# Performance work log

Hardware: AMD Instinct MI355X
Metric: run time of the kernel (lower is better)

The kernel has to match this reference:

```python
import jax, jax.numpy as jnp
import numpy as np

N_NODES = 50000
N_EDGES = 1600000
D_FEAT = 128
EPS = 1e-12  # matches F.normalize clamp_min eps


def setup_inputs() -> dict:
    key = jax.random.key(0)
    k1, k2 = jax.random.split(key)
    x = jax.random.normal(k1, (N_NODES, D_FEAT), dtype=jnp.float32)
    beta = jnp.ones((1,), dtype=jnp.float32)  # AGNNConv learnable scalar, init 1.0
    edge_index = jax.random.randint(k2, (2, N_EDGES), 0, N_NODES, dtype=jnp.int64)
    return {"x": x, "beta": beta, "edge_index": edge_index}


def reference(x, beta, edge_index):
    N = x.shape[0]
    # AGNNConv default add_self_loops=True
    loop = jnp.arange(N, dtype=edge_index.dtype)
    src = jnp.concatenate([edge_index[0], loop])  # j (source / message sender)
    dst = jnp.concatenate([edge_index[1], loop])  # i (target / aggregator)

    # cosine-similarity attention logits per edge, scaled by beta
    xn = x * jax.lax.rsqrt(jnp.maximum(jnp.sum(x * x, axis=-1, keepdims=True), EPS * EPS))
    logits = beta[0] * jnp.sum(xn[src] * xn[dst], axis=-1)  # [E+N]

    # segment softmax over incoming edges of each target node
    m = jax.ops.segment_max(logits, dst, num_segments=N)
    m = jax.lax.stop_gradient(m)
    e = jnp.exp(logits - m[dst])
    s = jax.ops.segment_sum(e, dst, num_segments=N)
    alpha = e / s[dst]  # self-loops guarantee s > 0

    # scatter-aggregate messages alpha_e * x_src
    out = jax.ops.segment_sum(alpha[:, None] * x[src], dst, num_segments=N)

    # wrapper: activation (relu); normalization=False; dropout p=0 -> identity
    return jax.nn.relu(out)
```

## Files before the change

### kernel.cpp

```cpp
#include <hip/hip_runtime.h>

#define NN 50000
#define NE 1600000
#define DF 128
#define NB 1250
#define BSZ 40
#define CAP 1664
#define NWGP 256
#define CHKP 6250
#define NBF 3125

typedef float v2f __attribute__((ext_vector_type(2)));
typedef float v4f __attribute__((ext_vector_type(4)));
typedef unsigned int v2u __attribute__((ext_vector_type(2)));

static __device__ __forceinline__ float bflo(unsigned int u) {
    unsigned int v = u << 16; float f; __builtin_memcpy(&f, &v, 4); return f;
}
static __device__ __forceinline__ float bfhi(unsigned int u) {
    unsigned int v = u & 0xFFFF0000u; float f; __builtin_memcpy(&f, &v, 4); return f;
}
static __device__ __forceinline__ unsigned int f2bf(float f) {
    unsigned int u; __builtin_memcpy(&u, &f, 4);
    u += 0x7FFFu + ((u >> 16) & 1u);
    return u >> 16;
}
static __device__ __forceinline__ v4f cvt4_i8(unsigned int u) {
    v4f r;
    r.x = (float)(int)(signed char)(u);
    r.y = (float)(int)(signed char)(u >> 8);
    r.z = (float)(int)(signed char)(u >> 16);
    r.w = (float)(int)(signed char)(u >> 24);
    return r;
}
static __device__ __forceinline__ v2f pk_fma(v2f a, v2f b, v2f c) {
    v2f d;
    asm("v_pk_fma_f32 %0, %1, %2, %3" : "=v"(d) : "v"(a), "v"(b), "0"(c));
    return d;
}
static __device__ __forceinline__ v2f pk_mul(v2f a, v2f b) {
    v2f d;
    asm("v_pk_mul_f32 %0, %1, %2" : "=v"(d) : "v"(a), "v"(b));
    return d;
}
static __device__ __forceinline__ v2f pk_add(v2f a, v2f b) {
    v2f d;
    asm("v_pk_add_f32 %0, %1, %2" : "=v"(d) : "v"(a), "v"(b));
    return d;
}

static __device__ __forceinline__ int block_excl_scan512(int v, int t, int* wsum8) {
    int lane = t & 63, wv = t >> 6;
    int s = v;
    #pragma unroll
    for (int off = 1; off < 64; off <<= 1) {
        int u = __shfl_up(s, off);
        if (lane >= off) s += u;
    }
    if (lane == 63) wsum8[wv] = s;
    __syncthreads();
    int add = 0;
    #pragma unroll
    for (int w = 0; w < 8; ++w) add += (w < wv) ? wsum8[w] : 0;
    __syncthreads();
    return s + add - v;
}

static __device__ __forceinline__ int block_excl_scan256(int v, int t, int* wsum4) {
    int lane = t & 63, wv = t >> 6;
    int s = v;
    #pragma unroll
    for (int off = 1; off < 64; off <<= 1) {
        int u = __shfl_up(s, off);
        if (lane >= off) s += u;
    }
    if (lane == 63) wsum4[wv] = s;
    __syncthreads();
    int add = 0;
    #pragma unroll
    for (int w = 0; w < 4; ++w) add += (w < wv) ? wsum4[w] : 0;
    __syncthreads();
    return s + add - v;
}

__global__ __launch_bounds__(512)
void k_norm_part(const float* __restrict__ x,
                 const int* __restrict__ ei,
                 unsigned int* __restrict__ xq,
                 float* __restrict__ norm,
                 unsigned int* __restrict__ sn,
                 unsigned int* __restrict__ descG,
                 unsigned int* __restrict__ pairs) {
    __shared__ int wsum8[8];
    __shared__ int cntL[NB];
    __shared__ int offL[NB];
    __shared__ unsigned int stg[CHKP];
    int t = threadIdx.x;
    if (blockIdx.x >= NWGP) {
        int l32 = t & 31;
        int node = (blockIdx.x - NWGP) * 16 + (t >> 5);
        float4 v = ((const float4*)(x + (size_t)node * DF))[l32];
        float ss = v.x * v.x + v.y * v.y + v.z * v.z + v.w * v.w;
        float am = fmaxf(fmaxf(fabsf(v.x), fabsf(v.y)), fmaxf(fabsf(v.z), fabsf(v.w)));
        #pragma unroll
        for (int m = 1; m < 32; m <<= 1) {
            ss += __shfl_xor(ss, m);
            am = fmaxf(am, __shfl_xor(am, m));
        }
        float rinv = rsqrtf(fmaxf(ss, 1e-24f));
        am = fmaxf(am, 1e-30f);
        float qsc = 127.0f / am;
        int q0 = (int)rintf(v.x * qsc);
        int q1 = (int)rintf(v.y * qsc);
        int q2 = (int)rintf(v.z * qsc);
        int q3 = (int)rintf(v.w * qsc);
        unsigned int u = (q0 & 255) | ((q1 & 255) << 8) | ((q2 & 255) << 16)
                       | ((unsigned int)q3 << 24);
        xq[(size_t)node * 32 + l32] = u;
        if (l32 == 0) {
            float m = am * (1.0f / 127.0f);
            float s = rinv * m;
            norm[node] = ss * rinv;
            sn[node] = (f2bf(m) << 16) | f2bf(s);
        }
        return;
    }
    int wg = blockIdx.x;
    const int* srcp = ei + wg * CHKP;
    const int* dstp = ei + NE + wg * CHKP;
    for (int i = t; i < NB; i += 512) cntL[i] = 0;
    __syncthreads();
    #pragma unroll 4
    for (int i = t; i < CHKP; i += 512) atomicAdd(&cntL[dstp[i] / BSZ], 1);
    __syncthreads();
    {
        int base = t * 3;
        int loc[3];
        int s = 0;
        #pragma unroll
        for (int q = 0; q < 3; ++q) {
            int idx = base + q;
            int v = (idx < NB) ? cntL[idx] : 0;
            loc[q] = s;
            s += v;
        }
        int ex = block_excl_scan512(s, t, wsum8);
        #pragma unroll
        for (int q = 0; q < 3; ++q) {
            int idx = base + q;
            if (idx < NB) offL[idx] = ex + loc[q];
        }
    }
    __syncthreads();
    for (int i = t; i < NB; i += 512)
        descG[(size_t)wg * NB + i] = ((unsigned int)offL[i] << 16) | (unsigned int)cntL[i];
    __syncthreads();
    #pragma unroll 2
    for (int i = t; i < CHKP; i += 512) {
        int src = srcp[i];
        int dst = dstp[i];
        int b = dst / BSZ;
        int pos = atomicAdd(&offL[b], 1);
        stg[pos] = ((unsigned int)(dst - b * BSZ) << 16) | (unsigned int)src;
    }
    __syncthreads();
    unsigned int* chunk = pairs + (size_t)wg * CHKP;
    #pragma unroll 4
    for (int i = t; i < CHKP; i += 512) chunk[i] = stg[i];
}

__global__ __launch_bounds__(256)
void k_build_gather(const unsigned int* __restrict__ xq,
                    const unsigned int* __restrict__ sn,
                    const float* __restrict__ norm,
                    const unsigned int* __restrict__ descG,
                    const unsigned int* __restrict__ pairs,
                    const float* __restrict__ beta_p,
                    float* __restrict__ out) {
    __shared__ int wsum4[4];
    __shared__ int lenS[NWGP], offS[NWGP], rbase[NWGP];
    __shared__ unsigned int rawL[CAP];
    __shared__ unsigned int colSrc[CAP];
    __shared__ unsigned int colSN[CAP];
    __shared__ int hist[BSZ];
    __shared__ int rp[BSZ + 1];
    __shared__ int stot;
    int b = blockIdx.x, t = threadIdx.x;

    {
        unsigned int d = descG[(size_t)t * NB + b];
        int len = (int)(d & 0xFFFFu);
        int ex = block_excl_scan256(len, t, wsum4);
        lenS[t] = len;
        offS[t] = (int)(d >> 16);
        rbase[t] = ex;
        if (t == 255) stot = ex + len;
    }
    if (t < BSZ) hist[t] = 0;
    __syncthreads();
    int cnt = stot;
    if (cnt > CAP) cnt = CAP;

    int g8 = t >> 3, l8 = t & 7;
    for (int r = g8; r < NWGP; r += 32) {
        int len = lenS[r];
        int rb = rbase[r];
        const unsigned int* sp = pairs + (size_t)r * CHKP + offS[r];
        for (int q = l8; q < len; q += 8) {
            int pos = rb + q;
            if (pos < CAP) rawL[pos] = sp[q];
        }
    }
    __syncthreads();
    for (int i = t; i < cnt; i += 256) atomicAdd(&hist[rawL[i] >> 16], 1);
    __syncthreads();
    if (t < 64) {
        int v = (t < BSZ) ? hist[t] : 0;
        int s = v;
        #pragma unroll
        for (int off = 1; off < 64; off <<= 1) {
            int u = __shfl_up(s, off);
            if (t >= off) s += u;
        }
        if (t < BSZ) { rp[t + 1] = s; hist[t] = s - v; }
        if (t == 0) rp[0] = 0;
    }
    __syncthreads();
    for (int i = t; i < cnt; i += 256) {
        unsigned int p = rawL[i];
        unsigned int src = p & 0xFFFFu;
        int pos = atomicAdd(&hist[p >> 16], 1);
        colSrc[pos] = src;
        colSN[pos] = sn[src];
    }
    __syncthreads();

    int lane = t & 63;
    int w = t >> 6;
    int j = lane & 15;
    int g = lane >> 4;
    float beta = beta_p[0];
    float c = -fabsf(beta);
    for (int ln = w; ln < BSZ; ln += 4) {
        int node = b * BSZ + ln;
        v2u du = ((const v2u*)(xq + (size_t)node * 32))[j];
        v4f c0 = cvt4_i8(du.x), c1 = cvt4_i8(du.y);
        v2f xd2[4];
        xd2[0].x = c0.x; xd2[0].y = c0.y;
        xd2[1].x = c0.z; xd2[1].y = c0.w;
        xd2[2].x = c1.x; xd2[2].y = c1.y;
        xd2[3].x = c1.z; xd2[3].y = c1.w;
        float sd = bflo(sn[node]);
        float ke = beta * sd;
        v2f acc2[4];
        #pragma unroll
        for (int q = 0; q < 4; ++q) { acc2[q].x = 0.f; acc2[q].y = 0.f; }
        float ssum = 0.f;
        int b0 = rp[ln], b1 = rp[ln + 1];

        int k = b0 + g;
        int kA = (k     < b1) ? k     : 0;
        int kB = (k + 4 < b1) ? k + 4 : 0;
        unsigned int srcA = colSrc[kA] & 0xFFFFu;
        unsigned int srcB = colSrc[kB] & 0xFFFFu;
        unsigned int snA = colSN[kA];
        unsigned int snB = colSN[kB];
        v2u rA = ((const v2u*)(xq + (size_t)srcA * 32))[j];
        v2u rB = ((const v2u*)(xq + (size_t)srcB * 32))[j];

        for (; k < b1; k += 8) {
            int kC = (k +  8 < b1) ? k +  8 : 0;
            int kD = (k + 12 < b1) ? k + 12 : 0;
            unsigned int srcC = colSrc[kC] & 0xFFFFu;
            unsigned int srcD = colSrc[kD] & 0xFFFFu;
            unsigned int snC = colSN[kC];
            unsigned int snD = colSN[kD];
            v2u rC = ((const v2u*)(xq + (size_t)srcC * 32))[j];
            v2u rD = ((const v2u*)(xq + (size_t)srcD * 32))[j];

            v4f a0 = cvt4_i8(rA.x), a1 = cvt4_i8(rA.y);
            v4f b0v = cvt4_i8(rB.x), b1v = cvt4_i8(rB.y);
            v2f xsA[4], xsB[4];
            xsA[0].x = a0.x; xsA[0].y = a0.y;  xsA[1].x = a0.z; xsA[1].y = a0.w;
            xsA[2].x = a1.x; xsA[2].y = a1.y;  xsA[3].x = a1.z; xsA[3].y = a1.w;
            xsB[0].x = b0v.x; xsB[0].y = b0v.y; xsB[1].x = b0v.z; xsB[1].y = b0v.w;
            xsB[2].x = b1v.x; xsB[2].y = b1v.y; xsB[3].x = b1v.z; xsB[3].y = b1v.w;
            v2f dpA = pk_mul(xd2[0], xsA[0]);
            v2f dpB = pk_mul(xd2[0], xsB[0]);
            #pragma unroll
            for (int q = 1; q < 4; ++q) {
                dpA = pk_fma(xd2[q], xsA[q], dpA);
                dpB = pk_fma(xd2[q], xsB[q], dpB);
            }
            v2f dAB;
            dAB.x = dpA.x + dpA.y;
            dAB.y = dpB.x + dpB.y;
            #pragma unroll
            for (int m = 1; m < 16; m <<= 1) {
                v2f o;
                o.x = __shfl_xor(dAB.x, m);
                o.y = __shfl_xor(dAB.y, m);
                dAB = pk_add(dAB, o);
            }
            float eA = __expf(fmaf(ke * bflo(snA), dAB.x, c));
            float eB = __expf(fmaf(ke * bflo(snB), dAB.y, c));
            eB = (k + 4 < b1) ? eB : 0.f;
            ssum += eA + eB;
            float wA = eA * bfhi(snA);
            float wB = eB * bfhi(snB);
            v2f wA2; wA2.x = wA; wA2.y = wA;
            v2f wB2; wB2.x = wB; wB2.y = wB;
            #pragma unroll
            for (int q = 0; q < 4; ++q) {
                acc2[q] = pk_fma(wA2, xsA[q], acc2[q]);
                acc2[q] = pk_fma(wB2, xsB[q], acc2[q]);
            }
            srcA = srcC; srcB = srcD; snA = snC; snB = snD; rA = rC; rB = rD;
        }

        ssum += __shfl_xor(ssum, 16);
        ssum += __shfl_xor(ssum, 32);
        #pragma unroll
        for (int q = 0; q < 4; ++q) {
            v2f o;
            o.x = __shfl_xor(acc2[q].x, 16);
            o.y = __shfl_xor(acc2[q].y, 16);
            acc2[q] = pk_add(acc2[q], o);
            o.x = __shfl_xor(acc2[q].x, 32);
            o.y = __shfl_xor(acc2[q].y, 32);
            acc2[q] = pk_add(acc2[q], o);
        }
        float e_self = __expf(beta + c);
        ssum += e_self;
        float wsl = e_self * norm[node] * sd;
        v2f wsl2; wsl2.x = wsl; wsl2.y = wsl;
        #pragma unroll
        for (int q = 0; q < 4; ++q) acc2[q] = pk_fma(wsl2, xd2[q], acc2[q]);

        if (g == 0) {
            float inv = 1.0f / ssum;
            float4 o0, o1;
            o0.x = fmaxf(0.f, acc2[0].x * inv); o0.y = fmaxf(0.f, acc2[0].y * inv);
            o0.z = fmaxf(0.f, acc2[1].x * inv); o0.w = fmaxf(0.f, acc2[1].y * inv);
            o1.x = fmaxf(0.f, acc2[2].x * inv); o1.y = fmaxf(0.f, acc2[2].y * inv);
            o1.z = fmaxf(0.f, acc2[3].x * inv); o1.w = fmaxf(0.f, acc2[3].y * inv);
            float4* op = (float4*)(out + (size_t)node * DF + 8 * j);
            op[0] = o0;
            op[1] = o1;
        }
    }
}

extern "C" void kernel_launch(void* const* d_in, const int* in_sizes, int n_in,
                              void* d_out, int out_size, void* d_ws, size_t ws_size,
                              hipStream_t stream) {
    const float* x    = (const float*)d_in[0];
    const float* beta = (const float*)d_in[1];
    const int*   ei   = (const int*)d_in[2];
    float*       out  = (float*)d_out;

    char* ws = (char*)d_ws;
    unsigned int* xq    = (unsigned int*)ws;
    float*        norm  = (float*)(ws + 6400000);
    unsigned int* sn    = (unsigned int*)(ws + 6600000);
    unsigned int* descG = (unsigned int*)(ws + 6800000);
    unsigned int* pairs = (unsigned int*)(ws + 8080000);

    k_norm_part  <<<NWGP + NBF, 512, 0, stream>>>(x, ei, xq, norm, sn, descG, pairs);
    k_build_gather<<<NB,        256, 0, stream>>>(xq, sn, norm, descG, pairs, beta, out);
}
```

Baseline: 155.9 us.

## Use offset-unsigned int8 with udot4 dot products and deeper prefetch

Stores the quantized features as unsigned bytes offset by 128 and computes each edge dot product with the hardware udot4 instruction. The offset terms are corrected using a per-node row sum stored next to the scale pair, and a weighted-sum correction is applied to the aggregation. It also merges the norm and scale arrays into one packed uint2 and deepens the software prefetch from two to four edges ahead. The aim is to cut VALU work for conversion and dot products, at the cost of more registers, extra LDS and more correction arithmetic.

```diff
diff --git a/kernel.cpp b/kernel.cpp
--- a/kernel.cpp
+++ b/kernel.cpp
@@ -11,7 +11,6 @@
 #define NBF 3125
 
 typedef float v2f __attribute__((ext_vector_type(2)));
-typedef float v4f __attribute__((ext_vector_type(4)));
 typedef unsigned int v2u __attribute__((ext_vector_type(2)));
 
 static __device__ __forceinline__ float bflo(unsigned int u) {
@@ -25,13 +24,15 @@
     u += 0x7FFFu + ((u >> 16) & 1u);
     return u >> 16;
 }
-static __device__ __forceinline__ v4f cvt4_i8(unsigned int u) {
-    v4f r;
-    r.x = (float)(int)(signed char)(u);
-    r.y = (float)(int)(signed char)(u >> 8);
-    r.z = (float)(int)(signed char)(u >> 16);
-    r.w = (float)(int)(signed char)(u >> 24);
-    return r;
+static __device__ __forceinline__ void ub8(v2u r, v2f* f) {
+    f[0].x = (float)( r.x         & 255u);
+    f[0].y = (float)((r.x >>  8)  & 255u);
+    f[1].x = (float)((r.x >> 16)  & 255u);
+    f[1].y = (float)( r.x >> 24         );
+    f[2].x = (float)( r.y         & 255u);
+    f[2].y = (float)((r.y >>  8)  & 255u);
+    f[3].x = (float)((r.y >> 16)  & 255u);
+    f[3].y = (float)( r.y >> 24         );
 }
 static __device__ __forceinline__ v2f pk_fma(v2f a, v2f b, v2f c) {
     v2f d;
@@ -87,8 +88,7 @@
 void k_norm_part(const float* __restrict__ x,
                  const int* __restrict__ ei,
                  unsigned int* __restrict__ xq,
-                 float* __restrict__ norm,
-                 unsigned int* __restrict__ sn,
+                 uint2* __restrict__ snr,
                  unsigned int* __restrict__ descG,
                  unsigned int* __restrict__ pairs) {
     __shared__ int wsum8[8];
@@ -110,18 +110,24 @@
         float rinv = rsqrtf(fmaxf(ss, 1e-24f));
         am = fmaxf(am, 1e-30f);
         float qsc = 127.0f / am;
-        int q0 = (int)rintf(v.x * qsc);
-        int q1 = (int)rintf(v.y * qsc);
-        int q2 = (int)rintf(v.z * qsc);
-        int q3 = (int)rintf(v.w * qsc);
-        unsigned int u = (q0 & 255) | ((q1 & 255) << 8) | ((q2 & 255) << 16)
-                       | ((unsigned int)q3 << 24);
+        int q0 = (int)rintf(v.x * qsc) + 128;
+        int q1 = (int)rintf(v.y * qsc) + 128;
+        int q2 = (int)rintf(v.z * qsc) + 128;
+        int q3 = (int)rintf(v.w * qsc) + 128;
+        unsigned int u = (unsigned)q0 | ((unsigned)q1 << 8) | ((unsigned)q2 << 16)
+                       | ((unsigned)q3 << 24);
+        int rs = q0 + q1 + q2 + q3;
+        #pragma unroll
+        for (int m = 1; m < 32; m <<= 1) rs += __shfl_xor(rs, m);
         xq[(size_t)node * 32 + l32] = u;
         if (l32 == 0) {
-            float m = am * (1.0f / 127.0f);
-            float s = rinv * m;
-            norm[node] = ss * rinv;
-            sn[node] = (f2bf(m) << 16) | f2bf(s);
+            float mm = am * (1.0f / 127.0f);
+            float sv = rinv * mm;
+            uint2 p;
+            p.x = (f2bf(mm) << 16) | f2bf(sv);
+            float rsf = 128.0f * (float)rs;
+            __builtin_memcpy(&p.y, &rsf, 4);
+            snr[node] = p;
         }
         return;
     }
@@ -171,8 +177,7 @@
 
 __global__ __launch_bounds__(256)
 void k_build_gather(const unsigned int* __restrict__ xq,
-                    const unsigned int* __restrict__ sn,
-                    const float* __restrict__ norm,
+                    const uint2* __restrict__ snr,
                     const unsigned int* __restrict__ descG,
                     const unsigned int* __restrict__ pairs,
                     const float* __restrict__ beta_p,
@@ -181,7 +186,7 @@
     __shared__ int lenS[NWGP], offS[NWGP], rbase[NWGP];
     __shared__ unsigned int rawL[CAP];
     __shared__ unsigned int colSrc[CAP];
-    __shared__ unsigned int colSN[CAP];
+    __shared__ uint2 colSNR[CAP];
     __shared__ int hist[BSZ];
     __shared__ int rp[BSZ + 1];
     __shared__ int stot;
@@ -231,7 +236,7 @@
         unsigned int src = p & 0xFFFFu;
         int pos = atomicAdd(&hist[p >> 16], 1);
         colSrc[pos] = src;
-        colSN[pos] = sn[src];
+        colSNR[pos] = snr[src];
     }
     __syncthreads();
 
@@ -240,61 +245,73 @@
     int j = lane & 15;
     int g = lane >> 4;
     float beta = beta_p[0];
-    float c = -fabsf(beta);
+    float cc = -fabsf(beta);
+
+#define FETCH(KK, SNV, RSV, ROW) {                                      \
+        int kc_ = ((KK) < b1r) ? (KK) : 0;                              \
+        unsigned sv_ = colSrc[kc_] & 0xFFFFu;                           \
+        uint2 tt_ = colSNR[kc_];                                        \
+        SNV = tt_.x;                                                    \
+        __builtin_memcpy(&RSV, &tt_.y, 4);                              \
+        ROW = ((const v2u*)(xq + (size_t)sv_ * 32))[j];                 \
+    }
+
     for (int ln = w; ln < BSZ; ln += 4) {
         int node = b * BSZ + ln;
         v2u du = ((const v2u*)(xq + (size_t)node * 32))[j];
-        v4f c0 = cvt4_i8(du.x), c1 = cvt4_i8(du.y);
-        v2f xd2[4];
-        xd2[0].x = c0.x; xd2[0].y = c0.y;
-        xd2[1].x = c0.z; xd2[1].y = c0.w;
-        xd2[2].x = c1.x; xd2[2].y = c1.y;
-        xd2[3].x = c1.z; xd2[3].y = c1.w;
-        float sd = bflo(sn[node]);
-        float ke = beta * sd;
+        uint2 sd = snr[node];
+        float m_d = bfhi(sd.x);
+        float s_d = bflo(sd.x);
+        float rsd; __builtin_memcpy(&rsd, &sd.y, 4);
+        float Kd = 2097152.0f - rsd;
+        float ke = beta * s_d;
+        v2f xdf[4];
+        ub8(du, xdf);
         v2f acc2[4];
         #pragma unroll
         for (int q = 0; q < 4; ++q) { acc2[q].x = 0.f; acc2[q].y = 0.f; }
-        float ssum = 0.f;
-        int b0 = rp[ln], b1 = rp[ln + 1];
-
-        int k = b0 + g;
-        int kA = (k     < b1) ? k     : 0;
-        int kB = (k + 4 < b1) ? k + 4 : 0;
-        unsigned int srcA = colSrc[kA] & 0xFFFFu;
-        unsigned int srcB = colSrc[kB] & 0xFFFFu;
-        unsigned int snA = colSN[kA];
-        unsigned int snB = colSN[kB];
-        v2u rA = ((const v2u*)(xq + (size_t)srcA * 32))[j];
-        v2u rB = ((const v2u*)(xq + (size_t)srcB * 32))[j];
-
-        for (; k < b1; k += 8) {
-            int kC = (k +  8 < b1) ? k +  8 : 0;
-            int kD = (k + 12 < b1) ? k + 12 : 0;
-            unsigned int srcC = colSrc[kC] & 0xFFFFu;
-            unsigned int srcD = colSrc[kD] & 0xFFFFu;
-            unsigned int snC = colSN[kC];
-            unsigned int snD = colSN[kD];
-            v2u rC = ((const v2u*)(xq + (size_t)srcC * 32))[j];
-            v2u rD = ((const v2u*)(xq + (size_t)srcD * 32))[j];
-
-            v4f a0 = cvt4_i8(rA.x), a1 = cvt4_i8(rA.y);
-            v4f b0v = cvt4_i8(rB.x), b1v = cvt4_i8(rB.y);
-            v2f xsA[4], xsB[4];
-            xsA[0].x = a0.x; xsA[0].y = a0.y;  xsA[1].x = a0.z; xsA[1].y = a0.w;
-            xsA[2].x = a1.x; xsA[2].y = a1.y;  xsA[3].x = a1.z; xsA[3].y = a1.w;
-            xsB[0].x = b0v.x; xsB[0].y = b0v.y; xsB[1].x = b0v.z; xsB[1].y = b0v.w;
-            xsB[2].x = b1v.x; xsB[2].y = b1v.y; xsB[3].x = b1v.z; xsB[3].y = b1v.w;
-            v2f dpA = pk_mul(xd2[0], xsA[0]);
-            v2f dpB = pk_mul(xd2[0], xsB[0]);
-            #pragma unroll
-            for (int q = 1; q < 4; ++q) {
-                dpA = pk_fma(xd2[q], xsA[q], dpA);
-                dpB = pk_fma(xd2[q], xsB[q], dpB);
+        float ssum = 0.f, wsum = 0.f;
+        int b0r = rp[ln], b1r = rp[ln + 1];
+
+        int k = b0r + g;
+        unsigned snA, snB, snC, snD, snE, snF;
+        float rsA, rsB, rsC, rsD, rsE, rsF2;
+        v2u rA, rB, rC, rD, rE, rF;
+        FETCH(k,      snA, rsA, rA);
+        FETCH(k + 4,  snB, rsB, rB);
+        FETCH(k + 8,  snC, rsC, rC);
+        FETCH(k + 12, snD, rsD, rD);
+
+        for (; k < b1r; k += 8) {
+            FETCH(k + 16, snE, rsE, rE);
+            FETCH(k + 20, snF, rsF2, rF);
+
+            v2f faA[4], faB[4];
+            ub8(rA, faA);
+            ub8(rB, faB);
+            v2f dAB;
+#if __has_builtin(__builtin_amdgcn_udot4)
+            {
+                unsigned dA = __builtin_amdgcn_udot4(du.x, rA.x,
+                              __builtin_amdgcn_udot4(du.y, rA.y, 0u, false), false);
+                unsigned dB = __builtin_amdgcn_udot4(du.x, rB.x,
+                              __builtin_amdgcn_udot4(du.y, rB.y, 0u, false), false);
+                dAB.x = (float)dA;
+                dAB.y = (float)dB;
             }
-            v2f dAB;
-            dAB.x = dpA.x + dpA.y;
-            dAB.y = dpB.x + dpB.y;
+#else
+            {
+                v2f dpA = pk_mul(xdf[0], faA[0]);
+                v2f dpB = pk_mul(xdf[0], faB[0]);
+                #pragma unroll
+                for (int q = 1; q < 4; ++q) {
+                    dpA = pk_fma(xdf[q], faA[q], dpA);
+                    dpB = pk_fma(xdf[q], faB[q], dpB);
+                }
+                dAB.x = dpA.x + dpA.y;
+                dAB.y = dpB.x + dpB.y;
+            }
+#endif
             #pragma unroll
             for (int m = 1; m < 16; m <<= 1) {
                 v2f o;
@@ -302,24 +319,32 @@
                 o.y = __shfl_xor(dAB.y, m);
                 dAB = pk_add(dAB, o);
             }
-            float eA = __expf(fmaf(ke * bflo(snA), dAB.x, c));
-            float eB = __expf(fmaf(ke * bflo(snB), dAB.y, c));
-            eB = (k + 4 < b1) ? eB : 0.f;
-            ssum += eA + eB;
+            float dotA = dAB.x - rsA + Kd;
+            float dotB = dAB.y - rsB + Kd;
+            float eA = __expf(fmaf(ke * bflo(snA), dotA, cc));
+            float eB = __expf(fmaf(ke * bflo(snB), dotB, cc));
+            eB = (k + 4 < b1r) ? eB : 0.f;
             float wA = eA * bfhi(snA);
             float wB = eB * bfhi(snB);
+            ssum += eA + eB;
+            wsum += wA + wB;
             v2f wA2; wA2.x = wA; wA2.y = wA;
             v2f wB2; wB2.x = wB; wB2.y = wB;
             #pragma unroll
             for (int q = 0; q < 4; ++q) {
-                acc2[q] = pk_fma(wA2, xsA[q], acc2[q]);
-                acc2[q] = pk_fma(wB2, xsB[q], acc2[q]);
+                acc2[q] = pk_fma(wA2, faA[q], acc2[q]);
+                acc2[q] = pk_fma(wB2, faB[q], acc2[q]);
             }
-            srcA = srcC; srcB = srcD; snA = snC; snB = snD; rA = rC; rB = rD;
+            snA = snC; rsA = rsC; rA = rC;
+            snB = snD; rsB = rsD; rB = rD;
+            snC = snE; rsC = rsE; rC = rE;
+            snD = snF; rsD = rsF2; rD = rF;
         }
 
         ssum += __shfl_xor(ssum, 16);
         ssum += __shfl_xor(ssum, 32);
+        wsum += __shfl_xor(wsum, 16);
+        wsum += __shfl_xor(wsum, 32);
         #pragma unroll
         for (int q = 0; q < 4; ++q) {
             v2f o;
@@ -330,25 +355,32 @@
             o.y = __shfl_xor(acc2[q].y, 32);
             acc2[q] = pk_add(acc2[q], o);
         }
-        float e_self = __expf(beta + c);
+        float e_self = __expf(beta + cc);
         ssum += e_self;
-        float wsl = e_self * norm[node] * sd;
+        float wsl = e_self * m_d;
+        wsum += wsl;
         v2f wsl2; wsl2.x = wsl; wsl2.y = wsl;
         #pragma unroll
-        for (int q = 0; q < 4; ++q) acc2[q] = pk_fma(wsl2, xd2[q], acc2[q]);
+        for (int q = 0; q < 4; ++q) acc2[q] = pk_fma(wsl2, xdf[q], acc2[q]);
 
         if (g == 0) {
             float inv = 1.0f / ssum;
+            float w128 = 128.0f * wsum;
             float4 o0, o1;
-            o0.x = fmaxf(0.f, acc2[0].x * inv); o0.y = fmaxf(0.f, acc2[0].y * inv);
-            o0.z = fmaxf(0.f, acc2[1].x * inv); o0.w = fmaxf(0.f, acc2[1].y * inv);
-            o1.x = fmaxf(0.f, acc2[2].x * inv); o1.y = fmaxf(0.f, acc2[2].y * inv);
-            o1.z = fmaxf(0.f, acc2[3].x * inv); o1.w = fmaxf(0.f, acc2[3].y * inv);
+            o0.x = fmaxf(0.f, (acc2[0].x - w128) * inv);
+            o0.y = fmaxf(0.f, (acc2[0].y - w128) * inv);
+            o0.z = fmaxf(0.f, (acc2[1].x - w128) * inv);
+            o0.w = fmaxf(0.f, (acc2[1].y - w128) * inv);
+            o1.x = fmaxf(0.f, (acc2[2].x - w128) * inv);
+            o1.y = fmaxf(0.f, (acc2[2].y - w128) * inv);
+            o1.z = fmaxf(0.f, (acc2[3].x - w128) * inv);
+            o1.w = fmaxf(0.f, (acc2[3].y - w128) * inv);
             float4* op = (float4*)(out + (size_t)node * DF + 8 * j);
             op[0] = o0;
             op[1] = o1;
         }
     }
+#undef FETCH
 }
 
 extern "C" void kernel_launch(void* const* d_in, const int* in_sizes, int n_in,
@@ -361,11 +393,10 @@
 
     char* ws = (char*)d_ws;
     unsigned int* xq    = (unsigned int*)ws;
-    float*        norm  = (float*)(ws + 6400000);
-    unsigned int* sn    = (unsigned int*)(ws + 6600000);
-    unsigned int* descG = (unsigned int*)(ws + 6800000);
-    unsigned int* pairs = (unsigned int*)(ws + 8080000);
-
-    k_norm_part  <<<NWGP + NBF, 512, 0, stream>>>(x, ei, xq, norm, sn, descG, pairs);
-    k_build_gather<<<NB,        256, 0, stream>>>(xq, sn, norm, descG, pairs, beta, out);
-}
+    uint2*        snr   = (uint2*)(ws + 6400000);
+    unsigned int* descG = (unsigned int*)(ws + 7200000);
+    unsigned int* pairs = (unsigned int*)(ws + 8480000);
+
+    k_norm_part  <<<NWGP + NBF, 512, 0, stream>>>(x, ei, xq, snr, descG, pairs);
+    k_build_gather<<<NB,        256, 0, stream>>>(xq, snr, descG, pairs, beta, out);
+}
```

Measured after the change: 159.3 us. +2.2%, slower.
